# Optimization experiments

Measured on AMD Instinct MI355X. Metric: run time of the kernel, lower is better.

Reference implementation:

```python
import jax, jax.numpy as jnp
import numpy as np
from jax import lax

B, T, C, H, HOR = 64, 2048, 64, 256, 96
BETA, THR = 0.9, 1.0


def setup_inputs() -> dict:
    key = jax.random.key(0)
    ks = jax.random.split(key, 10)
    s = lambda *sh: 1.0 / np.sqrt(sh[-1])
    return {
        "x": jax.random.normal(ks[0], (B, T, C), jnp.float32),
        "snn_w": jax.random.uniform(ks[1], (H, C), jnp.float32, -s(C), s(C)),
        "snn_b": jax.random.uniform(ks[2], (H,), jnp.float32, -s(C), s(C)),
        "gru_wih": jax.random.uniform(ks[3], (3 * H, C + H), jnp.float32, -s(H), s(H)),
        "gru_whh": jax.random.uniform(ks[4], (3 * H, H), jnp.float32, -s(H), s(H)),
        "gru_bih": jax.random.uniform(ks[5], (3 * H,), jnp.float32, -s(H), s(H)),
        "gru_bhh": jax.random.uniform(ks[6], (3 * H,), jnp.float32, -s(H), s(H)),
        "head_w": jax.random.uniform(ks[7], (HOR, H), jnp.float32, -s(H), s(H)),
        "head_b": jax.random.uniform(ks[8], (HOR,), jnp.float32, -s(H), s(H)),
    }


@jax.custom_vjp
def spike(x):
    return (x > 0).astype(x.dtype)

def _spike_fwd(x):
    return spike(x), x

def _spike_bwd(x, g):
    # snntorch ATan surrogate, alpha=2: grad = 1 / (1 + (pi*x)^2)
    return (g / (1.0 + (jnp.pi * x) ** 2),)

spike.defvjp(_spike_fwd, _spike_bwd)


def reference(x, snn_w, snn_b, gru_wih, gru_whh, gru_bih, gru_bhh, head_w, head_b):
    # Batched SNN input current across all timesteps: [B,T,H]
    cur = jnp.einsum("btc,hc->bth", x, snn_w) + snn_b

    def lif_step(mem, i_t):
        # reset computed from previous mem, detached (snntorch mem_reset)
        reset = lax.stop_gradient((mem > THR).astype(mem.dtype))
        mem_new = BETA * mem + i_t - reset * THR
        spk = spike(mem_new - THR)
        return mem_new, spk

    mem0 = jnp.zeros((B, H), x.dtype)
    _, spks = lax.scan(lif_step, mem0, cur.transpose(1, 0, 2))  # [T,B,H]

    h_comb = jnp.concatenate([x, spks.transpose(1, 0, 2)], axis=-1)  # [B,T,C+H]

    # GRU: precompute input gates for all timesteps
    gx = jnp.einsum("btc,gc->btg", h_comb, gru_wih) + gru_bih  # [B,T,3H]

    def gru_step(h, gx_t):
        gh = h @ gru_whh.T + gru_bhh
        xr, xz, xn = jnp.split(gx_t, 3, axis=-1)
        hr, hz, hn = jnp.split(gh, 3, axis=-1)
        r = jax.nn.sigmoid(xr + hr)
        z = jax.nn.sigmoid(xz + hz)
        n = jnp.tanh(xn + r * hn)
        h_new = (1.0 - z) * n + z * h
        return h_new, None

    h0 = jnp.zeros((B, H), x.dtype)
    hT, _ = lax.scan(gru_step, h0, gx.transpose(1, 0, 2))

    return hT @ head_w.T + head_b  # [B, HOR]
```

## Files before the change

kernel.cpp:

```cpp
#include <hip/hip_runtime.h>
#include <cstdint>
#include <cstddef>

#define B_   64
#define T_   2048
#define C_   64
#define H_   256
#define G3_  768
#define HOR_ 96

typedef _Float16 h2 __attribute__((ext_vector_type(2)));
typedef _Float16 h8 __attribute__((ext_vector_type(8)));
typedef _Float16 f16x8 __attribute__((ext_vector_type(8)));
typedef float f32x4 __attribute__((ext_vector_type(4)));

#define K1_TT 128
__global__ __launch_bounds__(256) void k_cur(const float* __restrict__ x,
                                             const float* __restrict__ w,
                                             const float* __restrict__ bias,
                                             float* __restrict__ cur) {
  __shared__ float xs[K1_TT * C_];
  const int b = blockIdx.x;
  const int t0 = blockIdx.y * K1_TT;
  const int tid = threadIdx.x;

  const float4* xsrc = (const float4*)(x + ((size_t)b * T_ + t0) * C_);
  float4* xdst = (float4*)xs;
#pragma unroll
  for (int i = 0; i < (K1_TT * C_ / 4) / 256; i++)
    xdst[tid + i * 256] = xsrc[tid + i * 256];

  float wr[C_];
  const float4* wp = (const float4*)(w + (size_t)tid * C_);
#pragma unroll
  for (int q = 0; q < C_ / 4; q++) {
    float4 v = wp[q];
    wr[4 * q + 0] = v.x; wr[4 * q + 1] = v.y;
    wr[4 * q + 2] = v.z; wr[4 * q + 3] = v.w;
  }
  const float bb = bias[tid];
  __syncthreads();

  for (int t = 0; t < K1_TT; t++) {
    const float4* xrow = (const float4*)(xs + t * C_);
    float a0 = 0.f, a1 = 0.f;
#pragma unroll
    for (int q = 0; q < C_ / 4; q += 2) {
      float4 v0 = xrow[q];
      float4 v1 = xrow[q + 1];
      a0 += wr[4 * q + 0] * v0.x + wr[4 * q + 1] * v0.y +
            wr[4 * q + 2] * v0.z + wr[4 * q + 3] * v0.w;
      a1 += wr[4 * q + 4] * v1.x + wr[4 * q + 5] * v1.y +
            wr[4 * q + 6] * v1.z + wr[4 * q + 7] * v1.w;
    }
    cur[((size_t)b * T_ + t0 + t) * H_ + tid] = a0 + a1 + bb;
  }
}

__global__ __launch_bounds__(64) void k_lif(const float* __restrict__ cur,
                                            unsigned char* __restrict__ spk) {
  const int b = blockIdx.x >> 2;
  const int h = ((blockIdx.x & 3) << 6) + threadIdx.x;
  const float* cp = cur + (size_t)b * T_ * H_ + h;
  unsigned char* sp = spk + (size_t)b * T_ * H_ + h;
  float mem = 0.f;
#pragma unroll 8
  for (int t = 0; t < T_; t++) {
    float c = cp[(size_t)t * H_];
    float reset = (mem > 1.0f) ? 1.0f : 0.0f;
    mem = 0.9f * mem + c - reset;
    sp[(size_t)t * H_] = (mem > 1.0f) ? (unsigned char)1 : (unsigned char)0;
  }
}

#define GM 128
#define GN 128
#define AKP 40
#define CTP 136
__global__ __launch_bounds__(256) void k_gx(const float* __restrict__ x,
                                            const unsigned char* __restrict__ spk,
                                            const float* __restrict__ wih,
                                            const float* __restrict__ bih,
                                            _Float16* __restrict__ gx) {
  alignas(16) __shared__ _Float16 Ah[GM * AKP];
  alignas(16) __shared__ _Float16 Bh[GN * AKP];
  alignas(16) __shared__ _Float16 Ct[GM * CTP];
  const int tid = threadIdx.x;
  const int lane = tid & 63;
  const int wave = tid >> 6;
  const int ln = lane & 15;
  const int qd = lane >> 4;
  const int m0 = blockIdx.y * GM;
  const int n0 = blockIdx.x * GN;
  const int wm = (wave & 1) * 64;
  const int wn = (wave >> 1) * 64;

  f32x4 acc[4][4] = {};

  for (int kc = 0; kc < 10; kc++) {
    const int k0 = kc * 32;
    if (k0 < 64) {
#pragma unroll
      for (int i = 0; i < 4; i++) {
        int idx = tid + i * 256;
        int r = idx >> 3;
        int c4 = (idx & 7) * 4;
        float4 v = *(const float4*)(x + (size_t)(m0 + r) * C_ + k0 + c4);
        h2 lo, hi;
        lo.x = (_Float16)v.x; lo.y = (_Float16)v.y;
        hi.x = (_Float16)v.z; hi.y = (_Float16)v.w;
        h2* d = (h2*)&Ah[r * AKP + c4];
        d[0] = lo; d[1] = hi;
      }
    } else {
#pragma unroll
      for (int i = 0; i < 4; i++) {
        int idx = tid + i * 256;
        int r = idx >> 3;
        int c4 = (idx & 7) * 4;
        uchar4 u = *(const uchar4*)(spk + (size_t)(m0 + r) * H_ + (k0 - 64) + c4);
        h2 lo, hi;
        lo.x = (_Float16)(int)u.x; lo.y = (_Float16)(int)u.y;
        hi.x = (_Float16)(int)u.z; hi.y = (_Float16)(int)u.w;
        h2* d = (h2*)&Ah[r * AKP + c4];
        d[0] = lo; d[1] = hi;
      }
    }
#pragma unroll
    for (int i = 0; i < 4; i++) {
      int idx = tid + i * 256;
      int r = idx >> 3;
      int c4 = (idx & 7) * 4;
      float4 v = *(const float4*)(wih + (size_t)(n0 + r) * 320 + k0 + c4);
      h2 lo, hi;
      lo.x = (_Float16)v.x; lo.y = (_Float16)v.y;
      hi.x = (_Float16)v.z; hi.y = (_Float16)v.w;
      h2* d = (h2*)&Bh[r * AKP + c4];
      d[0] = lo; d[1] = hi;
    }
    __syncthreads();
    f16x8 a[4], bb[4];
#pragma unroll
    for (int mt = 0; mt < 4; mt++)
      a[mt] = *(const f16x8*)&Ah[(wm + mt * 16 + ln) * AKP + qd * 8];
#pragma unroll
    for (int nt = 0; nt < 4; nt++)
      bb[nt] = *(const f16x8*)&Bh[(wn + nt * 16 + ln) * AKP + qd * 8];
#pragma unroll
    for (int mt = 0; mt < 4; mt++)
#pragma unroll
      for (int nt = 0; nt < 4; nt++)
        acc[mt][nt] = __builtin_amdgcn_mfma_f32_16x16x32_f16(a[mt], bb[nt],
                                                             acc[mt][nt], 0, 0, 0);
    __syncthreads();
  }

  float bias[4];
#pragma unroll
  for (int nt = 0; nt < 4; nt++) bias[nt] = bih[n0 + wn + nt * 16 + ln];
#pragma unroll
  for (int mt = 0; mt < 4; mt++)
#pragma unroll
    for (int nt = 0; nt < 4; nt++) {
      int n = wn + nt * 16 + ln;
#pragma unroll
      for (int r = 0; r < 4; r++) {
        int m = wm + mt * 16 + qd * 4 + r;
        Ct[m * CTP + n] = (_Float16)(acc[mt][nt][r] + bias[nt]);
      }
    }
  __syncthreads();
#pragma unroll
  for (int i = 0; i < 8; i++) {
    int idx = tid + i * 256;
    int r = idx >> 4;
    int c = (idx & 15) * 8;
    *(h8*)(gx + (size_t)(m0 + r) * G3_ + n0 + c) = *(const h8*)&Ct[r * CTP + c];
  }
}

#define DQ_ (0.0625f / (127.0f * 127.0f))
__global__ __launch_bounds__(512) void k_gru(const _Float16* __restrict__ gx,
                                             const float* __restrict__ whh,
                                             const float* __restrict__ bhh,
                                             const float* __restrict__ head_w,
                                             const float* __restrict__ head_b,
                                             float* __restrict__ out) {
  const int b = blockIdx.x;
  const int tid = threadIdx.x;
  const int lane = tid & 63;
  const int wave = tid >> 6;
  const int j = wave * 32 + (lane >> 1);
  const int kq = lane & 1;
  const int k0 = kq * 128;

  alignas(16) __shared__ int hq[2][64];
  __shared__ float hbuf32[H_];

  int wr[32], wz[32], wn[32];
  {
    const float qs = 2032.0f;
    const float4* p0 = (const float4*)(whh + (size_t)j * H_ + k0);
    const float4* p1 = (const float4*)(whh + (size_t)(H_ + j) * H_ + k0);
    const float4* p2 = (const float4*)(whh + (size_t)(2 * H_ + j) * H_ + k0);
#pragma unroll
    for (int q = 0; q < 32; q++) {
      float4 a = p0[q];
      wr[q] = ((int)rintf(a.x * qs) & 255) | (((int)rintf(a.y * qs) & 255) << 8) |
              (((int)rintf(a.z * qs) & 255) << 16) | (((int)rintf(a.w * qs) & 255) << 24);
      float4 c = p1[q];
      wz[q] = ((int)rintf(c.x * qs) & 255) | (((int)rintf(c.y * qs) & 255) << 8) |
              (((int)rintf(c.z * qs) & 255) << 16) | (((int)rintf(c.w * qs) & 255) << 24);
      float4 d = p2[q];
      wn[q] = ((int)rintf(d.x * qs) & 255) | (((int)rintf(d.y * qs) & 255) << 8) |
              (((int)rintf(d.z * qs) & 255) << 16) | (((int)rintf(d.w * qs) & 255) << 24);
    }
  }
  const float br_ = bhh[j], bz_ = bhh[H_ + j], bn_ = bhh[2 * H_ + j];

  if (tid < 128) ((int*)hq)[tid] = 0;
  float hj = 0.f;
  __syncthreads();

  const _Float16* gxb = gx + (size_t)b * T_ * G3_;
  _Float16 pr = gxb[j], pz = gxb[H_ + j], pn = gxb[2 * H_ + j];

  int p = 0;
  for (int t = 0; t < T_; t++) {
    float xr = (float)pr, xz = (float)pz, xn = (float)pn;
    {
      int tn_ = (t + 1 < T_) ? t + 1 : t;
      const _Float16* g = gxb + (size_t)tn_ * G3_;
      pr = g[j]; pz = g[H_ + j]; pn = g[2 * H_ + j];
    }

    const int* hb = &hq[p][kq * 32];
    int ar = 0, az = 0, an = 0;
#pragma unroll
    for (int g4 = 0; g4 < 4; g4++) {
#pragma unroll
      for (int cc = 0; cc < 2; cc++) {
        int c = g4 * 2 + cc;
        int4 hv = *(const int4*)(hb + c * 4);
#pragma unroll
        for (int i = 0; i < 4; i++) {
          int h4 = (i == 0) ? hv.x : (i == 1) ? hv.y : (i == 2) ? hv.z : hv.w;
          int wi = c * 4 + i;
          ar = __builtin_amdgcn_sdot4(wr[wi], h4, ar, false);
          az = __builtin_amdgcn_sdot4(wz[wi], h4, az, false);
          an = __builtin_amdgcn_sdot4(wn[wi], h4, an, false);
        }
      }
      __builtin_amdgcn_sched_barrier(2 | 4 | 16 | 32 | 64);
    }
    ar += __shfl_xor(ar, 1, 64);
    az += __shfl_xor(az, 1, 64);
    an += __shfl_xor(an, 1, 64);

    float r = 1.f / (1.f + __expf(-(xr + (float)ar * DQ_ + br_)));
    float z = 1.f / (1.f + __expf(-(xz + (float)az * DQ_ + bz_)));
    float pre = xn + r * ((float)an * DQ_ + bn_);
    float e = __expf(2.f * pre);
    float n = 1.f - 2.f / (e + 1.f);
    hj = (1.f - z) * n + z * hj;

    if (kq == 0) ((char*)hq[p ^ 1])[j] = (char)(int)rintf(hj * 127.0f);
    p ^= 1;
    __syncthreads();
  }

  if (kq == 0) hbuf32[j] = hj;
  __syncthreads();

  if (tid < HOR_) {
    const float4* hw = (const float4*)(head_w + (size_t)tid * H_);
    const float4* hv4 = (const float4*)hbuf32;
    float acc = head_b[tid];
#pragma unroll
    for (int q = 0; q < H_ / 4; q++) {
      float4 w4 = hw[q];
      float4 v4 = hv4[q];
      acc += w4.x * v4.x + w4.y * v4.y + w4.z * v4.z + w4.w * v4.w;
    }
    out[(size_t)b * HOR_ + tid] = acc;
  }
}

extern "C" void kernel_launch(void* const* d_in, const int* in_sizes, int n_in,
                              void* d_out, int out_size, void* d_ws, size_t ws_size,
                              hipStream_t stream) {
  const float* x      = (const float*)d_in[0];
  const float* snn_w  = (const float*)d_in[1];
  const float* snn_b  = (const float*)d_in[2];
  const float* wih    = (const float*)d_in[3];
  const float* whh    = (const float*)d_in[4];
  const float* bih    = (const float*)d_in[5];
  const float* bhh    = (const float*)d_in[6];
  const float* head_w = (const float*)d_in[7];
  const float* head_b = (const float*)d_in[8];
  float* out = (float*)d_out;

  char* ws = (char*)d_ws;
  _Float16* gx = (_Float16*)ws;
  float* cur = (float*)ws;
  unsigned char* spk = (unsigned char*)(ws + (size_t)201326592);

  k_cur<<<dim3(B_, T_ / K1_TT), 256, 0, stream>>>(x, snn_w, snn_b, cur);
  k_lif<<<dim3(256), 64, 0, stream>>>(cur, spk);
  k_gx<<<dim3(G3_ / GN, (B_ * T_) / GM), 256, 0, stream>>>(x, spk, wih, bih, gx);
  k_gru<<<dim3(B_), 512, 0, stream>>>(gx, whh, bhh, head_w, head_b, out);
}
```

Baseline: 2.110 ms.

## Fuse input-gate GEMM with GRU recurrence via flag-based producer/consumer pipelining

Merges the gx GEMM and GRU scan into one persistent kernel. 64 blocks run the recurrence while 192 producer blocks compute gx in 128-timestep chunks per batch and signal completion with release atomics. Consumers spin on acquire loads before each chunk, so the GEMM overlaps with the serial recurrence. Producer blocks use only half their 512 threads, and the scheme needs all 256 blocks co-resident to avoid deadlock.

```diff
diff --git a/kernel.cpp b/kernel.cpp
--- a/kernel.cpp
+++ b/kernel.cpp
@@ -13,6 +13,8 @@
 typedef _Float16 h8 __attribute__((ext_vector_type(8)));
 typedef _Float16 f16x8 __attribute__((ext_vector_type(8)));
 typedef float f32x4 __attribute__((ext_vector_type(4)));
+
+__global__ void k_zero(int* __restrict__ flags) { flags[threadIdx.x] = 0; }
 
 #define K1_TT 128
 __global__ __launch_bounds__(256) void k_cur(const float* __restrict__ x,
@@ -77,125 +79,139 @@
 #define GN 128
 #define AKP 40
 #define CTP 136
-__global__ __launch_bounds__(256) void k_gx(const float* __restrict__ x,
-                                            const unsigned char* __restrict__ spk,
-                                            const float* __restrict__ wih,
-                                            const float* __restrict__ bih,
-                                            _Float16* __restrict__ gx) {
+#define DQ_ (0.0625f / (127.0f * 127.0f))
+__global__ __launch_bounds__(512) void k_fused(
+    const float* __restrict__ x, const unsigned char* __restrict__ spk,
+    const float* __restrict__ wih, const float* __restrict__ bih,
+    _Float16* __restrict__ gx, const float* __restrict__ whh,
+    const float* __restrict__ bhh, const float* __restrict__ head_w,
+    const float* __restrict__ head_b, float* __restrict__ out,
+    int* __restrict__ flags) {
   alignas(16) __shared__ _Float16 Ah[GM * AKP];
   alignas(16) __shared__ _Float16 Bh[GN * AKP];
   alignas(16) __shared__ _Float16 Ct[GM * CTP];
+  alignas(16) __shared__ int hq[2][64];
+  __shared__ float hbuf32[H_];
+
   const int tid = threadIdx.x;
   const int lane = tid & 63;
-  const int wave = tid >> 6;
-  const int ln = lane & 15;
-  const int qd = lane >> 4;
-  const int m0 = blockIdx.y * GM;
-  const int n0 = blockIdx.x * GN;
-  const int wm = (wave & 1) * 64;
-  const int wn = (wave >> 1) * 64;
-
-  f32x4 acc[4][4] = {};
-
-  for (int kc = 0; kc < 10; kc++) {
-    const int k0 = kc * 32;
-    if (k0 < 64) {
-#pragma unroll
-      for (int i = 0; i < 4; i++) {
-        int idx = tid + i * 256;
-        int r = idx >> 3;
-        int c4 = (idx & 7) * 4;
-        float4 v = *(const float4*)(x + (size_t)(m0 + r) * C_ + k0 + c4);
-        h2 lo, hi;
-        lo.x = (_Float16)v.x; lo.y = (_Float16)v.y;
-        hi.x = (_Float16)v.z; hi.y = (_Float16)v.w;
-        h2* d = (h2*)&Ah[r * AKP + c4];
-        d[0] = lo; d[1] = hi;
+
+  if (blockIdx.x >= 64) {
+    const int pidx = blockIdx.x - 64;
+    const int bb = pidx / 3;
+    const int pp = pidx - bb * 3;
+    const int wave = tid >> 6;
+    const int ln = lane & 15;
+    const int qd = lane >> 4;
+    const int wm = (wave & 1) * 64;
+    const int wn = ((wave >> 1) & 1) * 64;
+
+    for (int mt = 0; mt < 16; mt++) {
+      const int m0 = bb * 2048 + mt * 128;
+      for (int nh = 0; nh < 2; nh++) {
+        const int n0 = pp * 256 + nh * 128;
+        f32x4 acc[4][4] = {};
+        for (int kc = 0; kc < 10; kc++) {
+          const int k0 = kc * 32;
+          if (tid < 256) {
+            if (k0 < 64) {
+#pragma unroll
+              for (int i = 0; i < 4; i++) {
+                int idx = tid + i * 256;
+                int r = idx >> 3;
+                int c4 = (idx & 7) * 4;
+                float4 v = *(const float4*)(x + (size_t)(m0 + r) * C_ + k0 + c4);
+                h2 lo, hi;
+                lo.x = (_Float16)v.x; lo.y = (_Float16)v.y;
+                hi.x = (_Float16)v.z; hi.y = (_Float16)v.w;
+                h2* d = (h2*)&Ah[r * AKP + c4];
+                d[0] = lo; d[1] = hi;
+              }
+            } else {
+#pragma unroll
+              for (int i = 0; i < 4; i++) {
+                int idx = tid + i * 256;
+                int r = idx >> 3;
+                int c4 = (idx & 7) * 4;
+                uchar4 u = *(const uchar4*)(spk + (size_t)(m0 + r) * H_ + (k0 - 64) + c4);
+                h2 lo, hi;
+                lo.x = (_Float16)(int)u.x; lo.y = (_Float16)(int)u.y;
+                hi.x = (_Float16)(int)u.z; hi.y = (_Float16)(int)u.w;
+                h2* d = (h2*)&Ah[r * AKP + c4];
+                d[0] = lo; d[1] = hi;
+              }
+            }
+#pragma unroll
+            for (int i = 0; i < 4; i++) {
+              int idx = tid + i * 256;
+              int r = idx >> 3;
+              int c4 = (idx & 7) * 4;
+              float4 v = *(const float4*)(wih + (size_t)(n0 + r) * 320 + k0 + c4);
+              h2 lo, hi;
+              lo.x = (_Float16)v.x; lo.y = (_Float16)v.y;
+              hi.x = (_Float16)v.z; hi.y = (_Float16)v.w;
+              h2* d = (h2*)&Bh[r * AKP + c4];
+              d[0] = lo; d[1] = hi;
+            }
+          }
+          __syncthreads();
+          if (tid < 256) {
+            f16x8 a[4], bbf[4];
+#pragma unroll
+            for (int mtl = 0; mtl < 4; mtl++)
+              a[mtl] = *(const f16x8*)&Ah[(wm + mtl * 16 + ln) * AKP + qd * 8];
+#pragma unroll
+            for (int nt = 0; nt < 4; nt++)
+              bbf[nt] = *(const f16x8*)&Bh[(wn + nt * 16 + ln) * AKP + qd * 8];
+#pragma unroll
+            for (int mtl = 0; mtl < 4; mtl++)
+#pragma unroll
+              for (int nt = 0; nt < 4; nt++)
+                acc[mtl][nt] = __builtin_amdgcn_mfma_f32_16x16x32_f16(
+                    a[mtl], bbf[nt], acc[mtl][nt], 0, 0, 0);
+          }
+          __syncthreads();
+        }
+        if (tid < 256) {
+          float bias[4];
+#pragma unroll
+          for (int nt = 0; nt < 4; nt++) bias[nt] = bih[n0 + wn + nt * 16 + ln];
+#pragma unroll
+          for (int mtl = 0; mtl < 4; mtl++)
+#pragma unroll
+            for (int nt = 0; nt < 4; nt++) {
+              int n = wn + nt * 16 + ln;
+#pragma unroll
+              for (int r = 0; r < 4; r++) {
+                int m = wm + mtl * 16 + qd * 4 + r;
+                Ct[m * CTP + n] = (_Float16)(acc[mtl][nt][r] + bias[nt]);
+              }
+            }
+        }
+        __syncthreads();
+        if (tid < 256) {
+#pragma unroll
+          for (int i = 0; i < 8; i++) {
+            int idx = tid + i * 256;
+            int r = idx >> 4;
+            int c = (idx & 15) * 8;
+            *(h8*)(gx + (size_t)(m0 + r) * G3_ + n0 + c) = *(const h8*)&Ct[r * CTP + c];
+          }
+        }
+        __syncthreads();
       }
-    } else {
-#pragma unroll
-      for (int i = 0; i < 4; i++) {
-        int idx = tid + i * 256;
-        int r = idx >> 3;
-        int c4 = (idx & 7) * 4;
-        uchar4 u = *(const uchar4*)(spk + (size_t)(m0 + r) * H_ + (k0 - 64) + c4);
-        h2 lo, hi;
-        lo.x = (_Float16)(int)u.x; lo.y = (_Float16)(int)u.y;
-        hi.x = (_Float16)(int)u.z; hi.y = (_Float16)(int)u.w;
-        h2* d = (h2*)&Ah[r * AKP + c4];
-        d[0] = lo; d[1] = hi;
-      }
-    }
-#pragma unroll
-    for (int i = 0; i < 4; i++) {
-      int idx = tid + i * 256;
-      int r = idx >> 3;
-      int c4 = (idx & 7) * 4;
-      float4 v = *(const float4*)(wih + (size_t)(n0 + r) * 320 + k0 + c4);
-      h2 lo, hi;
-      lo.x = (_Float16)v.x; lo.y = (_Float16)v.y;
-      hi.x = (_Float16)v.z; hi.y = (_Float16)v.w;
-      h2* d = (h2*)&Bh[r * AKP + c4];
-      d[0] = lo; d[1] = hi;
-    }
-    __syncthreads();
-    f16x8 a[4], bb[4];
-#pragma unroll
-    for (int mt = 0; mt < 4; mt++)
-      a[mt] = *(const f16x8*)&Ah[(wm + mt * 16 + ln) * AKP + qd * 8];
-#pragma unroll
-    for (int nt = 0; nt < 4; nt++)
-      bb[nt] = *(const f16x8*)&Bh[(wn + nt * 16 + ln) * AKP + qd * 8];
-#pragma unroll
-    for (int mt = 0; mt < 4; mt++)
-#pragma unroll
-      for (int nt = 0; nt < 4; nt++)
-        acc[mt][nt] = __builtin_amdgcn_mfma_f32_16x16x32_f16(a[mt], bb[nt],
-                                                             acc[mt][nt], 0, 0, 0);
-    __syncthreads();
-  }
-
-  float bias[4];
-#pragma unroll
-  for (int nt = 0; nt < 4; nt++) bias[nt] = bih[n0 + wn + nt * 16 + ln];
-#pragma unroll
-  for (int mt = 0; mt < 4; mt++)
-#pragma unroll
-    for (int nt = 0; nt < 4; nt++) {
-      int n = wn + nt * 16 + ln;
-#pragma unroll
-      for (int r = 0; r < 4; r++) {
-        int m = wm + mt * 16 + qd * 4 + r;
-        Ct[m * CTP + n] = (_Float16)(acc[mt][nt][r] + bias[nt]);
-      }
-    }
-  __syncthreads();
-#pragma unroll
-  for (int i = 0; i < 8; i++) {
-    int idx = tid + i * 256;
-    int r = idx >> 4;
-    int c = (idx & 15) * 8;
-    *(h8*)(gx + (size_t)(m0 + r) * G3_ + n0 + c) = *(const h8*)&Ct[r * CTP + c];
-  }
-}
-
-#define DQ_ (0.0625f / (127.0f * 127.0f))
-__global__ __launch_bounds__(512) void k_gru(const _Float16* __restrict__ gx,
-                                             const float* __restrict__ whh,
-                                             const float* __restrict__ bhh,
-                                             const float* __restrict__ head_w,
-                                             const float* __restrict__ head_b,
-                                             float* __restrict__ out) {
+      if (tid == 0)
+        __hip_atomic_fetch_add(&flags[bb * 16 + mt], 1, __ATOMIC_RELEASE,
+                               __HIP_MEMORY_SCOPE_AGENT);
+    }
+    return;
+  }
+
   const int b = blockIdx.x;
-  const int tid = threadIdx.x;
-  const int lane = tid & 63;
   const int wave = tid >> 6;
   const int j = wave * 32 + (lane >> 1);
   const int kq = lane & 1;
   const int k0 = kq * 128;
-
-  alignas(16) __shared__ int hq[2][64];
-  __shared__ float hbuf32[H_];
 
   int wr[32], wz[32], wn[32];
   {
@@ -223,50 +239,59 @@
   __syncthreads();
 
   const _Float16* gxb = gx + (size_t)b * T_ * G3_;
-  _Float16 pr = gxb[j], pz = gxb[H_ + j], pn = gxb[2 * H_ + j];
-
   int p = 0;
-  for (int t = 0; t < T_; t++) {
-    float xr = (float)pr, xz = (float)pz, xn = (float)pn;
-    {
-      int tn_ = (t + 1 < T_) ? t + 1 : t;
-      const _Float16* g = gxb + (size_t)tn_ * G3_;
-      pr = g[j]; pz = g[H_ + j]; pn = g[2 * H_ + j];
-    }
-
-    const int* hb = &hq[p][kq * 32];
-    int ar = 0, az = 0, an = 0;
-#pragma unroll
-    for (int g4 = 0; g4 < 4; g4++) {
-#pragma unroll
-      for (int cc = 0; cc < 2; cc++) {
-        int c = g4 * 2 + cc;
-        int4 hv = *(const int4*)(hb + c * 4);
-#pragma unroll
-        for (int i = 0; i < 4; i++) {
-          int h4 = (i == 0) ? hv.x : (i == 1) ? hv.y : (i == 2) ? hv.z : hv.w;
-          int wi = c * 4 + i;
-          ar = __builtin_amdgcn_sdot4(wr[wi], h4, ar, false);
-          az = __builtin_amdgcn_sdot4(wz[wi], h4, az, false);
-          an = __builtin_amdgcn_sdot4(wn[wi], h4, an, false);
+  for (int mt = 0; mt < 16; mt++) {
+    if (tid == 0) {
+      while (__hip_atomic_load(&flags[b * 16 + mt], __ATOMIC_ACQUIRE,
+                               __HIP_MEMORY_SCOPE_AGENT) < 3)
+        __builtin_amdgcn_s_sleep(8);
+    }
+    __syncthreads();
+
+    const _Float16* gc = gxb + (size_t)mt * 128 * G3_;
+    _Float16 pr = gc[j], pz = gc[H_ + j], pn = gc[2 * H_ + j];
+
+    for (int tt = 0; tt < 128; tt++) {
+      float xr = (float)pr, xz = (float)pz, xn = (float)pn;
+      if (tt < 127) {
+        const _Float16* g = gc + (size_t)(tt + 1) * G3_;
+        pr = g[j]; pz = g[H_ + j]; pn = g[2 * H_ + j];
+      }
+
+      const int* hb = &hq[p][kq * 32];
+      int ar = 0, az = 0, an = 0;
+#pragma unroll
+      for (int g4 = 0; g4 < 4; g4++) {
+#pragma unroll
+        for (int cc = 0; cc < 2; cc++) {
+          int c = g4 * 2 + cc;
+          int4 hv = *(const int4*)(hb + c * 4);
+#pragma unroll
+          for (int i = 0; i < 4; i++) {
+            int h4 = (i == 0) ? hv.x : (i == 1) ? hv.y : (i == 2) ? hv.z : hv.w;
+            int wi = c * 4 + i;
+            ar = __builtin_amdgcn_sdot4(wr[wi], h4, ar, false);
+            az = __builtin_amdgcn_sdot4(wz[wi], h4, az, false);
+            an = __builtin_amdgcn_sdot4(wn[wi], h4, an, false);
+          }
         }
+        __builtin_amdgcn_sched_barrier(2 | 4 | 16 | 32 | 64);
       }
-      __builtin_amdgcn_sched_barrier(2 | 4 | 16 | 32 | 64);
-    }
-    ar += __shfl_xor(ar, 1, 64);
-    az += __shfl_xor(az, 1, 64);
-    an += __shfl_xor(an, 1, 64);
-
-    float r = 1.f / (1.f + __expf(-(xr + (float)ar * DQ_ + br_)));
-    float z = 1.f / (1.f + __expf(-(xz + (float)az * DQ_ + bz_)));
-    float pre = xn + r * ((float)an * DQ_ + bn_);
-    float e = __expf(2.f * pre);
-    float n = 1.f - 2.f / (e + 1.f);
-    hj = (1.f - z) * n + z * hj;
-
-    if (kq == 0) ((char*)hq[p ^ 1])[j] = (char)(int)rintf(hj * 127.0f);
-    p ^= 1;
-    __syncthreads();
+      ar += __shfl_xor(ar, 1, 64);
+      az += __shfl_xor(az, 1, 64);
+      an += __shfl_xor(an, 1, 64);
+
+      float r = 1.f / (1.f + __expf(-(xr + (float)ar * DQ_ + br_)));
+      float z = 1.f / (1.f + __expf(-(xz + (float)az * DQ_ + bz_)));
+      float pre = xn + r * ((float)an * DQ_ + bn_);
+      float e = __expf(2.f * pre);
+      float n = 1.f - 2.f / (e + 1.f);
+      hj = (1.f - z) * n + z * hj;
+
+      if (kq == 0) ((char*)hq[p ^ 1])[j] = (char)(int)rintf(hj * 127.0f);
+      p ^= 1;
+      __syncthreads();
+    }
   }
 
   if (kq == 0) hbuf32[j] = hj;
@@ -304,9 +329,11 @@
   _Float16* gx = (_Float16*)ws;
   float* cur = (float*)ws;
   unsigned char* spk = (unsigned char*)(ws + (size_t)201326592);
-
+  int* flags = (int*)(ws + (size_t)234881024);
+
+  k_zero<<<1, 1024, 0, stream>>>(flags);
   k_cur<<<dim3(B_, T_ / K1_TT), 256, 0, stream>>>(x, snn_w, snn_b, cur);
   k_lif<<<dim3(256), 64, 0, stream>>>(cur, spk);
-  k_gx<<<dim3(G3_ / GN, (B_ * T_) / GM), 256, 0, stream>>>(x, spk, wih, bih, gx);
-  k_gru<<<dim3(B_), 512, 0, stream>>>(gx, whh, bhh, head_w, head_b, out);
+  k_fused<<<dim3(256), 512, 0, stream>>>(x, spk, wih, bih, gx, whh, bhh,
+                                         head_w, head_b, out, flags);
 }
```

Measured after the change: 1.995 ms. -5.5%, faster.
